# Kernel optimization log

Measured on AMD Instinct MI355X. Metric: run time of the kernel, lower is better.

## Reference

```python
import jax, jax.numpy as jnp
import numpy as np

N, S, D = 4, 2048, 1024
H, HD = 16, 64
DF = 3 * D
EPS = 1e-5

def _layernorm(x, g, b):
    mu = jnp.mean(x, axis=-1, keepdims=True)
    var = jnp.mean((x - mu) ** 2, axis=-1, keepdims=True)
    return (x - mu) * jax.lax.rsqrt(var + EPS) * g + b

def _pos_embed(s, d, dtype):
    pos = jnp.arange(s, dtype=dtype)                      # (S,)
    i = jnp.arange(d, dtype=dtype)                        # (D,)
    ang = pos[:, None] / (10000.0 ** (2.0 * i / d))       # (S,D)
    pe = jnp.where((jnp.arange(d) % 2) == 0, jnp.sin(ang), jnp.cos(ang))
    return pe

def setup_inputs() -> dict:
    key = jax.random.key(0)
    ks = jax.random.split(key, 12)
    def w(k, shape, fan_in):
        return jax.random.normal(k, shape, dtype=jnp.float32) * (fan_in ** -0.5)
    return {
        "x":  jax.random.normal(ks[0], (N, S, D), dtype=jnp.float32),
        "Wq": w(ks[1], (D, H * HD), D),
        "Wk": w(ks[2], (D, H * HD), D),
        "Wv": w(ks[3], (D, H * HD), D),
        "Wo": w(ks[4], (H * HD, D), H * HD),
        "W1": w(ks[5], (D, DF), D),
        "b1": jnp.zeros((DF,), dtype=jnp.float32),
        "W2": w(ks[6], (DF, D), DF),
        "b2": jnp.zeros((D,), dtype=jnp.float32),
        "g1": jnp.ones((D,), dtype=jnp.float32),
        "be1": jnp.zeros((D,), dtype=jnp.float32),
        "g2": jnp.ones((D,), dtype=jnp.float32),
        "be2": jnp.zeros((D,), dtype=jnp.float32),
    }

def reference(x, Wq, Wk, Wv, Wo, W1, b1, W2, b2, g1, be1, g2, be2):
    n, s, d = x.shape
    # positional encoding (added to x; note original scales scores by model_dim**0.5)
    x = x + _pos_embed(s, d, x.dtype)[None, :, :]
    # MHA on norm1(x)
    h = _layernorm(x, g1, be1)
    q = (h @ Wq).reshape(n, s, H, HD)
    k = (h @ Wk).reshape(n, s, H, HD)
    v = (h @ Wv).reshape(n, s, H, HD)
    scores = jnp.einsum('bqhd,bkhd->bhqk', q, k) / jnp.sqrt(jnp.asarray(d, x.dtype))
    attn = jax.nn.softmax(scores, axis=-1)
    o = jnp.einsum('bhqk,bkhd->bqhd', attn, v).reshape(n, s, H * HD)
    x = x + o @ Wo
    # FFN on norm2(x): Linear -> LeakyReLU(0.01) -> Linear (dropout = identity in eval)
    h2 = _layernorm(x, g2, be2)
    f = jax.nn.leaky_relu(h2 @ W1 + b1, negative_slope=0.01)
    x = x + (f @ W2 + b2)
    return x
```

## Files before the change

### kernel.cpp

```cpp
#include <hip/hip_runtime.h>

typedef unsigned short u16;
typedef __bf16 bf16x8 __attribute__((ext_vector_type(8)));
typedef float f32x4 __attribute__((ext_vector_type(4)));

__device__ __forceinline__ u16 f2bf(float f) {
  unsigned u = __builtin_bit_cast(unsigned, f);
  u += 0x7FFFu + ((u >> 16) & 1u);
  return (u16)(u >> 16);
}

#define GLOAD16(g, l) __builtin_amdgcn_global_load_lds( \
    (const __attribute__((address_space(1))) unsigned int*)(const void*)(g), \
    (__attribute__((address_space(3))) unsigned int*)(void*)(l), 16, 0, 0)

#define SW(r, c) (((r) << 6) + ((((c) ^ ((r) & 7))) << 3))

#define QSCALE 0.045084222393f

__global__ __launch_bounds__(256) void tconv(const float* __restrict__ W,
                                             u16* __restrict__ Wt, int K, int N) {
  __shared__ float t[32][33];
  int n0 = blockIdx.x * 32, k0 = blockIdx.y * 32;
  int tx = threadIdx.x, ty = threadIdx.y;
#pragma unroll
  for (int j = 0; j < 4; ++j)
    t[ty + j * 8][tx] = W[(size_t)(k0 + ty + j * 8) * N + n0 + tx];
  __syncthreads();
#pragma unroll
  for (int j = 0; j < 4; ++j)
    Wt[(size_t)(n0 + ty + j * 8) * K + k0 + tx] = f2bf(t[tx][ty + j * 8]);
}

template <bool PE>
__global__ __launch_bounds__(256) void ln_row(const float* __restrict__ in,
                                              const float* __restrict__ g,
                                              const float* __restrict__ be,
                                              float* __restrict__ xout,
                                              u16* __restrict__ hout) {
  const int row = blockIdx.x;
  const int tid = threadIdx.x;
  const int s = row & 2047;
  float4 xv = *(const float4*)&in[(size_t)row * 1024 + tid * 4];
  float vals[4];
  const float* xp = (const float*)&xv;
#pragma unroll
  for (int j = 0; j < 4; ++j) {
    float v = xp[j];
    if (PE) {
      int d = tid * 4 + j;
      float freq = powf(10000.f, -2.f * (float)d * (1.f / 1024.f));
      float ang = (float)s * freq;
      v += (d & 1) ? cosf(ang) : sinf(ang);
    }
    vals[j] = v;
  }
  if (PE) {
    float4 st;
    float* sp = (float*)&st;
#pragma unroll
    for (int j = 0; j < 4; ++j) sp[j] = vals[j];
    *(float4*)&xout[(size_t)row * 1024 + tid * 4] = st;
  }
  float sum = vals[0] + vals[1] + vals[2] + vals[3];
  float sq = vals[0] * vals[0] + vals[1] * vals[1] + vals[2] * vals[2] + vals[3] * vals[3];
#pragma unroll
  for (int d = 1; d < 64; d <<= 1) {
    sum += __shfl_xor(sum, d);
    sq += __shfl_xor(sq, d);
  }
  __shared__ float red[8];
  int wave = tid >> 6, lane = tid & 63;
  if (lane == 0) { red[wave] = sum; red[4 + wave] = sq; }
  __syncthreads();
  sum = red[0] + red[1] + red[2] + red[3];
  sq = red[4] + red[5] + red[6] + red[7];
  float mu = sum * (1.f / 1024.f);
  float var = sq * (1.f / 1024.f) - mu * mu;
  float rv = rsqrtf(var + 1e-5f);
#pragma unroll
  for (int j = 0; j < 4; ++j) {
    int d = tid * 4 + j;
    hout[(size_t)row * 1024 + d] = f2bf((vals[j] - mu) * rv * g[d] + be[d]);
  }
}

#define EPI_QKV 0
#define EPI_OPROJ 1
#define EPI_FFN1 2
#define EPI_FFN2 3

template <int EPI>
__global__ __launch_bounds__(256, 4) void gemm_bt(
    const u16* __restrict__ A, const u16* __restrict__ Bt, int M, int N, int K,
    const float* __restrict__ bias, const float* __restrict__ resid,
    float* __restrict__ outf, u16* __restrict__ outb,
    u16* __restrict__ oq, u16* __restrict__ okk, u16* __restrict__ ovt) {
  __shared__ __align__(16) u16 As[128 * 64];
  __shared__ __align__(16) u16 Bs[128 * 64];
  const int tid = threadIdx.x;
  const int wave = tid >> 6, lane = tid & 63;
  const int m0 = blockIdx.y * 128, n0 = blockIdx.x * 128;
  const int lrow = lane & 15, lhi = lane >> 4;
  const int wr = (wave >> 1) * 64, wc = (wave & 1) * 64;
  const int srow = tid >> 3;
  const int swsrc = ((tid & 7) ^ (srow & 7)) * 8;
  const u16* Ag = A + (size_t)(m0 + srow) * K + swsrc;
  const u16* Bg = Bt + (size_t)(n0 + srow) * K + swsrc;

  f32x4 acc[4][4] = {};

  for (int kt = 0; kt < K; kt += 64) {
#pragma unroll
    for (int j = 0; j < 4; ++j) {
      GLOAD16(Ag + (size_t)(j * 32) * K + kt, &As[j * 2048 + wave * 512]);
      GLOAD16(Bg + (size_t)(j * 32) * K + kt, &Bs[j * 2048 + wave * 512]);
    }
    __syncthreads();
    bf16x8 af[2][4], bfr[2][4];
#pragma unroll
    for (int kk = 0; kk < 2; ++kk) {
#pragma unroll
      for (int m = 0; m < 4; ++m)
        af[kk][m] = *(const bf16x8*)&As[SW(wr + m * 16 + lrow, kk * 4 + lhi)];
#pragma unroll
      for (int n = 0; n < 4; ++n)
        bfr[kk][n] = *(const bf16x8*)&Bs[SW(wc + n * 16 + lrow, kk * 4 + lhi)];
    }
#pragma unroll
    for (int kk = 0; kk < 2; ++kk)
#pragma unroll
      for (int m = 0; m < 4; ++m)
#pragma unroll
        for (int n = 0; n < 4; ++n)
          acc[m][n] = __builtin_amdgcn_mfma_f32_16x16x32_bf16(af[kk][m], bfr[kk][n], acc[m][n], 0, 0, 0);
    __syncthreads();
  }

#pragma unroll
  for (int m = 0; m < 4; ++m) {
#pragma unroll
    for (int n = 0; n < 4; ++n) {
#pragma unroll
      for (int i = 0; i < 4; ++i) {
        int row = m0 + wr + m * 16 + lhi * 4 + i;
        int col = n0 + wc + n * 16 + lrow;
        float v = acc[m][n][i];
        if (EPI == EPI_QKV) {
          int which = col >> 10, c = col & 1023;
          int h = c >> 6, hd = c & 63;
          int b = row >> 11, s = row & 2047;
          size_t qk = (((size_t)(b * 16 + h) * 2048 + s) << 6) + hd;
          if (which == 0) oq[qk] = f2bf(v * QSCALE);
          else if (which == 1) okk[qk] = f2bf(v);
          else ovt[((size_t)(b * 16 + h) * 64 + hd) * 2048 + s] = f2bf(v);
        } else if (EPI == EPI_OPROJ) {
          size_t idx = (size_t)row * 1024 + col;
          outf[idx] = v + resid[idx];
        } else if (EPI == EPI_FFN1) {
          float t = v + bias[col];
          t = t > 0.f ? t : 0.01f * t;
          outb[(size_t)row * 3072 + col] = f2bf(t);
        } else {
          size_t idx = (size_t)row * 1024 + col;
          outf[idx] = v + bias[col] + resid[idx];
        }
      }
    }
  }
}

__global__ __launch_bounds__(256, 3) void attn_fwd(const u16* __restrict__ qb,
                                                   const u16* __restrict__ kbuf,
                                                   const u16* __restrict__ vtb,
                                                   u16* __restrict__ ob) {
  __shared__ __align__(16) u16 Kl[2][64 * 64];
  __shared__ __align__(16) u16 Vl[2][64 * 64];
  __shared__ __align__(16) u16 Pl[128 * 64];
  const int tid = threadIdx.x, wave = tid >> 6, lane = tid & 63;
  const int wid = (blockIdx.x & 7) * 128 + (blockIdx.x >> 3);
  const int bh = wid >> 4, qt = wid & 15;
  const int lrow = lane & 15, lhi = lane >> 4;
  const u16* Qg = qb + (((size_t)bh * 2048 + qt * 128) << 6);
  const u16* Kg = kbuf + ((size_t)bh * 2048 << 6);
  const u16* Vg = vtb + (size_t)bh * 64 * 2048;
  const int srow = tid >> 3;
  const int swsrc = ((tid & 7) ^ (srow & 7)) * 8;

#pragma unroll
  for (int j = 0; j < 4; ++j)
    GLOAD16(Qg + (size_t)(srow + j * 32) * 64 + swsrc, &Pl[j * 2048 + wave * 512]);
#pragma unroll
  for (int j = 0; j < 2; ++j) {
    int r = srow + j * 32;
    GLOAD16(Kg + (size_t)r * 64 + swsrc, &Kl[0][j * 2048 + wave * 512]);
    GLOAD16(Vg + (size_t)r * 2048 + swsrc, &Vl[0][j * 2048 + wave * 512]);
  }
  __syncthreads();

  bf16x8 qf[2][2];
#pragma unroll
  for (int m = 0; m < 2; ++m)
#pragma unroll
    for (int kk = 0; kk < 2; ++kk)
      qf[m][kk] = *(const bf16x8*)&Pl[SW(wave * 32 + m * 16 + lrow, kk * 4 + lhi)];

  f32x4 oacc[2][4] = {};
  float lsum[8];
#pragma unroll
  for (int i = 0; i < 8; ++i) lsum[i] = 0.f;

  int cur = 0;
  for (int kv = 0; kv < 2048; kv += 64) {
    if (kv) __syncthreads();
    if (kv + 64 < 2048) {
#pragma unroll
      for (int j = 0; j < 2; ++j) {
        int r = srow + j * 32;
        GLOAD16(Kg + (size_t)(kv + 64 + r) * 64 + swsrc, &Kl[cur ^ 1][j * 2048 + wave * 512]);
        GLOAD16(Vg + (size_t)r * 2048 + kv + 64 + swsrc, &Vl[cur ^ 1][j * 2048 + wave * 512]);
      }
    }

    f32x4 sf[2][4] = {};
#pragma unroll
    for (int n = 0; n < 4; ++n) {
#pragma unroll
      for (int kk = 0; kk < 2; ++kk) {
        bf16x8 kf = *(const bf16x8*)&Kl[cur][SW(n * 16 + lrow, kk * 4 + lhi)];
        sf[0][n] = __builtin_amdgcn_mfma_f32_16x16x32_bf16(qf[0][kk], kf, sf[0][n], 0, 0, 0);
        sf[1][n] = __builtin_amdgcn_mfma_f32_16x16x32_bf16(qf[1][kk], kf, sf[1][n], 0, 0, 0);
      }
    }
#pragma unroll
    for (int m = 0; m < 2; ++m) {
#pragma unroll
      for (int i = 0; i < 4; ++i) {
        float rs = 0.f;
#pragma unroll
        for (int n = 0; n < 4; ++n) {
          float p = exp2f(sf[m][n][i]);
          sf[m][n][i] = p;
          rs += p;
        }
        lsum[m * 4 + i] += rs;
      }
    }
#pragma unroll
    for (int m = 0; m < 2; ++m)
#pragma unroll
      for (int n = 0; n < 4; ++n)
#pragma unroll
        for (int i = 0; i < 4; ++i) {
          int pr = wave * 32 + m * 16 + lhi * 4 + i;
          Pl[SW(pr, n * 2 + (lrow >> 3)) + (lrow & 7)] = f2bf(sf[m][n][i]);
        }
#pragma unroll
    for (int kk = 0; kk < 2; ++kk) {
      bf16x8 pf0 = *(const bf16x8*)&Pl[SW(wave * 32 + 0 + lrow, kk * 4 + lhi)];
      bf16x8 pf1 = *(const bf16x8*)&Pl[SW(wave * 32 + 16 + lrow, kk * 4 + lhi)];
#pragma unroll
      for (int n = 0; n < 4; ++n) {
        bf16x8 vf = *(const bf16x8*)&Vl[cur][SW(n * 16 + lrow, kk * 4 + lhi)];
        oacc[0][n] = __builtin_amdgcn_mfma_f32_16x16x32_bf16(pf0, vf, oacc[0][n], 0, 0, 0);
        oacc[1][n] = __builtin_amdgcn_mfma_f32_16x16x32_bf16(pf1, vf, oacc[1][n], 0, 0, 0);
      }
    }
    cur ^= 1;
  }

#pragma unroll
  for (int idx = 0; idx < 8; ++idx)
#pragma unroll
    for (int d = 1; d < 16; d <<= 1)
      lsum[idx] += __shfl_xor(lsum[idx], d, 16);

  const int b = bh >> 4, h = bh & 15;
#pragma unroll
  for (int m = 0; m < 2; ++m)
#pragma unroll
    for (int i = 0; i < 4; ++i) {
      int qrow = qt * 128 + wave * 32 + m * 16 + lhi * 4 + i;
      float inv = 1.f / lsum[m * 4 + i];
#pragma unroll
      for (int n = 0; n < 4; ++n) {
        int hd = n * 16 + lrow;
        ob[((size_t)(b * 2048 + qrow)) * 1024 + h * 64 + hd] = f2bf(oacc[m][n][i] * inv);
      }
    }
}

extern "C" void kernel_launch(void* const* d_in, const int* in_sizes, int n_in,
                              void* d_out, int out_size, void* d_ws, size_t ws_size,
                              hipStream_t stream) {
  const float* x = (const float*)d_in[0];
  const float* Wq = (const float*)d_in[1];
  const float* Wk = (const float*)d_in[2];
  const float* Wv = (const float*)d_in[3];
  const float* Wo = (const float*)d_in[4];
  const float* W1 = (const float*)d_in[5];
  const float* b1 = (const float*)d_in[6];
  const float* W2 = (const float*)d_in[7];
  const float* b2 = (const float*)d_in[8];
  const float* g1 = (const float*)d_in[9];
  const float* be1 = (const float*)d_in[10];
  const float* g2 = (const float*)d_in[11];
  const float* be2 = (const float*)d_in[12];

  char* ws = (char*)d_ws;
  const size_t MB = 1024 * 1024;
  float* x1 = (float*)(ws + 0);
  u16* h = (u16*)(ws + 32 * MB);
  u16* q = (u16*)(ws + 48 * MB);
  u16* k = (u16*)(ws + 64 * MB);
  u16* vt = (u16*)(ws + 80 * MB);
  u16* o = (u16*)(ws + 96 * MB);
  u16* f = (u16*)(ws + 48 * MB);
  u16* wqkv = (u16*)(ws + 112 * MB);
  u16* wo = (u16*)(ws + 118 * MB);
  u16* w1t = (u16*)(ws + 120 * MB);
  u16* w2t = (u16*)(ws + 126 * MB);
  float* out = (float*)d_out;

  dim3 tb(32, 8);
  tconv<<<dim3(32, 32), tb, 0, stream>>>(Wq, wqkv, 1024, 1024);
  tconv<<<dim3(32, 32), tb, 0, stream>>>(Wk, wqkv + 1024 * 1024, 1024, 1024);
  tconv<<<dim3(32, 32), tb, 0, stream>>>(Wv, wqkv + 2 * 1024 * 1024, 1024, 1024);
  tconv<<<dim3(32, 32), tb, 0, stream>>>(Wo, wo, 1024, 1024);
  tconv<<<dim3(96, 32), tb, 0, stream>>>(W1, w1t, 1024, 3072);
  tconv<<<dim3(32, 96), tb, 0, stream>>>(W2, w2t, 3072, 1024);

  ln_row<true><<<8192, 256, 0, stream>>>(x, g1, be1, x1, h);

  gemm_bt<EPI_QKV><<<dim3(24, 64), 256, 0, stream>>>(h, wqkv, 8192, 3072, 1024,
                                                     nullptr, nullptr, nullptr, nullptr,
                                                     q, k, vt);
  attn_fwd<<<1024, 256, 0, stream>>>(q, k, vt, o);

  gemm_bt<EPI_OPROJ><<<dim3(8, 64), 256, 0, stream>>>(o, wo, 8192, 1024, 1024,
                                                      nullptr, x1, x1, nullptr,
                                                      nullptr, nullptr, nullptr);
  ln_row<false><<<8192, 256, 0, stream>>>(x1, g2, be2, nullptr, h);

  gemm_bt<EPI_FFN1><<<dim3(24, 64), 256, 0, stream>>>(h, w1t, 8192, 3072, 1024,
                                                      b1, nullptr, nullptr, f,
                                                      nullptr, nullptr, nullptr);
  gemm_bt<EPI_FFN2><<<dim3(8, 64), 256, 0, stream>>>(f, w2t, 8192, 1024, 3072,
                                                     b2, x1, out, nullptr,
                                                     nullptr, nullptr, nullptr);
}
```

Measured before the change: 455.0 us.

## Merge weight transposes into one launch and process two query tiles per attention block

The six weight-transpose launches become a single kernel that picks the matrix from the block index, which cuts launch overhead. The attention kernel now runs 512 blocks that each loop over two query tiles, so fewer workgroups are launched and each stays resident longer. The exp2f with a log2e-folded QSCALE is replaced by __expf with QSCALE set to 1/32, which is the same maths written another way. With only 512 blocks, the attention launch may leave compute units underfilled or unbalanced.

```diff
diff --git a/kernel.cpp b/kernel.cpp
--- a/kernel.cpp
+++ b/kernel.cpp
@@ -16,12 +16,36 @@
 
 #define SW(r, c) (((r) << 6) + ((((c) ^ ((r) & 7))) << 3))
 
-#define QSCALE 0.045084222393f
-
-__global__ __launch_bounds__(256) void tconv(const float* __restrict__ W,
-                                             u16* __restrict__ Wt, int K, int N) {
+#define QSCALE 0.03125f
+
+__global__ __launch_bounds__(256) void tconv_all(
+    const float* __restrict__ Wq, const float* __restrict__ Wk,
+    const float* __restrict__ Wv, const float* __restrict__ Wo,
+    const float* __restrict__ W1, const float* __restrict__ W2,
+    u16* __restrict__ wqkv, u16* __restrict__ wo,
+    u16* __restrict__ w1t, u16* __restrict__ w2t) {
   __shared__ float t[32][33];
-  int n0 = blockIdx.x * 32, k0 = blockIdx.y * 32;
+  const int b = blockIdx.x;
+  const float* W;
+  u16* Wt;
+  int K, N, n0, k0;
+  if (b < 4096) {
+    int which = b >> 10, tt = b & 1023;
+    K = 1024; N = 1024;
+    n0 = (tt & 31) * 32; k0 = (tt >> 5) * 32;
+    W = (which == 0) ? Wq : (which == 1) ? Wk : (which == 2) ? Wv : Wo;
+    Wt = (which < 3) ? (wqkv + (size_t)which * 1024 * 1024) : wo;
+  } else if (b < 7168) {
+    int tt = b - 4096;
+    K = 1024; N = 3072;
+    n0 = (tt % 96) * 32; k0 = (tt / 96) * 32;
+    W = W1; Wt = w1t;
+  } else {
+    int tt = b - 7168;
+    K = 3072; N = 1024;
+    n0 = (tt & 31) * 32; k0 = (tt >> 5) * 32;
+    W = W2; Wt = w2t;
+  }
   int tx = threadIdx.x, ty = threadIdx.y;
 #pragma unroll
   for (int j = 0; j < 4; ++j)
@@ -178,116 +202,121 @@
   __shared__ __align__(16) u16 Vl[2][64 * 64];
   __shared__ __align__(16) u16 Pl[128 * 64];
   const int tid = threadIdx.x, wave = tid >> 6, lane = tid & 63;
-  const int wid = (blockIdx.x & 7) * 128 + (blockIdx.x >> 3);
-  const int bh = wid >> 4, qt = wid & 15;
+  const int wid = (blockIdx.x & 7) * 64 + (blockIdx.x >> 3);
+  const int bh = wid >> 3, qtb = wid & 7;
   const int lrow = lane & 15, lhi = lane >> 4;
-  const u16* Qg = qb + (((size_t)bh * 2048 + qt * 128) << 6);
   const u16* Kg = kbuf + ((size_t)bh * 2048 << 6);
   const u16* Vg = vtb + (size_t)bh * 64 * 2048;
   const int srow = tid >> 3;
   const int swsrc = ((tid & 7) ^ (srow & 7)) * 8;
-
-#pragma unroll
-  for (int j = 0; j < 4; ++j)
-    GLOAD16(Qg + (size_t)(srow + j * 32) * 64 + swsrc, &Pl[j * 2048 + wave * 512]);
-#pragma unroll
-  for (int j = 0; j < 2; ++j) {
-    int r = srow + j * 32;
-    GLOAD16(Kg + (size_t)r * 64 + swsrc, &Kl[0][j * 2048 + wave * 512]);
-    GLOAD16(Vg + (size_t)r * 2048 + swsrc, &Vl[0][j * 2048 + wave * 512]);
-  }
-  __syncthreads();
-
-  bf16x8 qf[2][2];
-#pragma unroll
-  for (int m = 0; m < 2; ++m)
-#pragma unroll
-    for (int kk = 0; kk < 2; ++kk)
-      qf[m][kk] = *(const bf16x8*)&Pl[SW(wave * 32 + m * 16 + lrow, kk * 4 + lhi)];
-
-  f32x4 oacc[2][4] = {};
-  float lsum[8];
-#pragma unroll
-  for (int i = 0; i < 8; ++i) lsum[i] = 0.f;
-
-  int cur = 0;
-  for (int kv = 0; kv < 2048; kv += 64) {
-    if (kv) __syncthreads();
-    if (kv + 64 < 2048) {
-#pragma unroll
-      for (int j = 0; j < 2; ++j) {
-        int r = srow + j * 32;
-        GLOAD16(Kg + (size_t)(kv + 64 + r) * 64 + swsrc, &Kl[cur ^ 1][j * 2048 + wave * 512]);
-        GLOAD16(Vg + (size_t)r * 2048 + kv + 64 + swsrc, &Vl[cur ^ 1][j * 2048 + wave * 512]);
-      }
-    }
-
-    f32x4 sf[2][4] = {};
-#pragma unroll
-    for (int n = 0; n < 4; ++n) {
+  const int b = bh >> 4, h = bh & 15;
+
+  for (int qi = 0; qi < 2; ++qi) {
+    const int qt = qtb + qi * 8;
+    const u16* Qg = qb + (((size_t)bh * 2048 + qt * 128) << 6);
+    if (qi) __syncthreads();
+
+#pragma unroll
+    for (int j = 0; j < 4; ++j)
+      GLOAD16(Qg + (size_t)(srow + j * 32) * 64 + swsrc, &Pl[j * 2048 + wave * 512]);
+#pragma unroll
+    for (int j = 0; j < 2; ++j) {
+      int r = srow + j * 32;
+      GLOAD16(Kg + (size_t)r * 64 + swsrc, &Kl[0][j * 2048 + wave * 512]);
+      GLOAD16(Vg + (size_t)r * 2048 + swsrc, &Vl[0][j * 2048 + wave * 512]);
+    }
+    __syncthreads();
+
+    bf16x8 qf[2][2];
+#pragma unroll
+    for (int m = 0; m < 2; ++m)
+#pragma unroll
+      for (int kk = 0; kk < 2; ++kk)
+        qf[m][kk] = *(const bf16x8*)&Pl[SW(wave * 32 + m * 16 + lrow, kk * 4 + lhi)];
+
+    f32x4 oacc[2][4] = {};
+    float lsum[8];
+#pragma unroll
+    for (int i = 0; i < 8; ++i) lsum[i] = 0.f;
+
+    int cur = 0;
+    for (int kv = 0; kv < 2048; kv += 64) {
+      if (kv) __syncthreads();
+      if (kv + 64 < 2048) {
+#pragma unroll
+        for (int j = 0; j < 2; ++j) {
+          int r = srow + j * 32;
+          GLOAD16(Kg + (size_t)(kv + 64 + r) * 64 + swsrc, &Kl[cur ^ 1][j * 2048 + wave * 512]);
+          GLOAD16(Vg + (size_t)r * 2048 + kv + 64 + swsrc, &Vl[cur ^ 1][j * 2048 + wave * 512]);
+        }
+      }
+
+      f32x4 sf[2][4] = {};
+#pragma unroll
+      for (int n = 0; n < 4; ++n) {
+#pragma unroll
+        for (int kk = 0; kk < 2; ++kk) {
+          bf16x8 kf = *(const bf16x8*)&Kl[cur][SW(n * 16 + lrow, kk * 4 + lhi)];
+          sf[0][n] = __builtin_amdgcn_mfma_f32_16x16x32_bf16(qf[0][kk], kf, sf[0][n], 0, 0, 0);
+          sf[1][n] = __builtin_amdgcn_mfma_f32_16x16x32_bf16(qf[1][kk], kf, sf[1][n], 0, 0, 0);
+        }
+      }
+#pragma unroll
+      for (int m = 0; m < 2; ++m) {
+#pragma unroll
+        for (int i = 0; i < 4; ++i) {
+          float rs = 0.f;
+#pragma unroll
+          for (int n = 0; n < 4; ++n) {
+            float p = __expf(sf[m][n][i]);
+            sf[m][n][i] = p;
+            rs += p;
+          }
+          lsum[m * 4 + i] += rs;
+        }
+      }
+#pragma unroll
+      for (int m = 0; m < 2; ++m)
+#pragma unroll
+        for (int n = 0; n < 4; ++n)
+#pragma unroll
+          for (int i = 0; i < 4; ++i) {
+            int pr = wave * 32 + m * 16 + lhi * 4 + i;
+            Pl[SW(pr, n * 2 + (lrow >> 3)) + (lrow & 7)] = f2bf(sf[m][n][i]);
+          }
 #pragma unroll
       for (int kk = 0; kk < 2; ++kk) {
-        bf16x8 kf = *(const bf16x8*)&Kl[cur][SW(n * 16 + lrow, kk * 4 + lhi)];
-        sf[0][n] = __builtin_amdgcn_mfma_f32_16x16x32_bf16(qf[0][kk], kf, sf[0][n], 0, 0, 0);
-        sf[1][n] = __builtin_amdgcn_mfma_f32_16x16x32_bf16(qf[1][kk], kf, sf[1][n], 0, 0, 0);
-      }
-    }
-#pragma unroll
-    for (int m = 0; m < 2; ++m) {
+        bf16x8 pf0 = *(const bf16x8*)&Pl[SW(wave * 32 + 0 + lrow, kk * 4 + lhi)];
+        bf16x8 pf1 = *(const bf16x8*)&Pl[SW(wave * 32 + 16 + lrow, kk * 4 + lhi)];
+#pragma unroll
+        for (int n = 0; n < 4; ++n) {
+          bf16x8 vf = *(const bf16x8*)&Vl[cur][SW(n * 16 + lrow, kk * 4 + lhi)];
+          oacc[0][n] = __builtin_amdgcn_mfma_f32_16x16x32_bf16(pf0, vf, oacc[0][n], 0, 0, 0);
+          oacc[1][n] = __builtin_amdgcn_mfma_f32_16x16x32_bf16(pf1, vf, oacc[1][n], 0, 0, 0);
+        }
+      }
+      cur ^= 1;
+    }
+
+#pragma unroll
+    for (int idx = 0; idx < 8; ++idx)
+#pragma unroll
+      for (int d = 1; d < 16; d <<= 1)
+        lsum[idx] += __shfl_xor(lsum[idx], d, 16);
+
+#pragma unroll
+    for (int m = 0; m < 2; ++m)
 #pragma unroll
       for (int i = 0; i < 4; ++i) {
-        float rs = 0.f;
+        int qrow = qt * 128 + wave * 32 + m * 16 + lhi * 4 + i;
+        float inv = 1.f / lsum[m * 4 + i];
 #pragma unroll
         for (int n = 0; n < 4; ++n) {
-          float p = exp2f(sf[m][n][i]);
-          sf[m][n][i] = p;
-          rs += p;
-        }
-        lsum[m * 4 + i] += rs;
-      }
-    }
-#pragma unroll
-    for (int m = 0; m < 2; ++m)
-#pragma unroll
-      for (int n = 0; n < 4; ++n)
-#pragma unroll
-        for (int i = 0; i < 4; ++i) {
-          int pr = wave * 32 + m * 16 + lhi * 4 + i;
-          Pl[SW(pr, n * 2 + (lrow >> 3)) + (lrow & 7)] = f2bf(sf[m][n][i]);
-        }
-#pragma unroll
-    for (int kk = 0; kk < 2; ++kk) {
-      bf16x8 pf0 = *(const bf16x8*)&Pl[SW(wave * 32 + 0 + lrow, kk * 4 + lhi)];
-      bf16x8 pf1 = *(const bf16x8*)&Pl[SW(wave * 32 + 16 + lrow, kk * 4 + lhi)];
-#pragma unroll
-      for (int n = 0; n < 4; ++n) {
-        bf16x8 vf = *(const bf16x8*)&Vl[cur][SW(n * 16 + lrow, kk * 4 + lhi)];
-        oacc[0][n] = __builtin_amdgcn_mfma_f32_16x16x32_bf16(pf0, vf, oacc[0][n], 0, 0, 0);
-        oacc[1][n] = __builtin_amdgcn_mfma_f32_16x16x32_bf16(pf1, vf, oacc[1][n], 0, 0, 0);
-      }
-    }
-    cur ^= 1;
-  }
-
-#pragma unroll
-  for (int idx = 0; idx < 8; ++idx)
-#pragma unroll
-    for (int d = 1; d < 16; d <<= 1)
-      lsum[idx] += __shfl_xor(lsum[idx], d, 16);
-
-  const int b = bh >> 4, h = bh & 15;
-#pragma unroll
-  for (int m = 0; m < 2; ++m)
-#pragma unroll
-    for (int i = 0; i < 4; ++i) {
-      int qrow = qt * 128 + wave * 32 + m * 16 + lhi * 4 + i;
-      float inv = 1.f / lsum[m * 4 + i];
-#pragma unroll
-      for (int n = 0; n < 4; ++n) {
-        int hd = n * 16 + lrow;
-        ob[((size_t)(b * 2048 + qrow)) * 1024 + h * 64 + hd] = f2bf(oacc[m][n][i] * inv);
-      }
-    }
+          int hd = n * 16 + lrow;
+          ob[((size_t)(b * 2048 + qrow)) * 1024 + h * 64 + hd] = f2bf(oacc[m][n][i] * inv);
+        }
+      }
+  }
 }
 
 extern "C" void kernel_launch(void* const* d_in, const int* in_sizes, int n_in,
@@ -322,20 +351,15 @@
   u16* w2t = (u16*)(ws + 126 * MB);
   float* out = (float*)d_out;
 
-  dim3 tb(32, 8);
-  tconv<<<dim3(32, 32), tb, 0, stream>>>(Wq, wqkv, 1024, 1024);
-  tconv<<<dim3(32, 32), tb, 0, stream>>>(Wk, wqkv + 1024 * 1024, 1024, 1024);
-  tconv<<<dim3(32, 32), tb, 0, stream>>>(Wv, wqkv + 2 * 1024 * 1024, 1024, 1024);
-  tconv<<<dim3(32, 32), tb, 0, stream>>>(Wo, wo, 1024, 1024);
-  tconv<<<dim3(96, 32), tb, 0, stream>>>(W1, w1t, 1024, 3072);
-  tconv<<<dim3(32, 96), tb, 0, stream>>>(W2, w2t, 3072, 1024);
+  tconv_all<<<10240, dim3(32, 8), 0, stream>>>(Wq, Wk, Wv, Wo, W1, W2,
+                                               wqkv, wo, w1t, w2t);
 
   ln_row<true><<<8192, 256, 0, stream>>>(x, g1, be1, x1, h);
 
   gemm_bt<EPI_QKV><<<dim3(24, 64), 256, 0, stream>>>(h, wqkv, 8192, 3072, 1024,
                                                      nullptr, nullptr, nullptr, nullptr,
                                                      q, k, vt);
-  attn_fwd<<<1024, 256, 0, stream>>>(q, k, vt, o);
+  attn_fwd<<<512, 256, 0, stream>>>(q, k, vt, o);
 
   gemm_bt<EPI_OPROJ><<<dim3(8, 64), 256, 0, stream>>>(o, wo, 8192, 1024, 1024,
                                                       nullptr, x1, x1, nullptr,
```

After: 434.3 us. -4.5%, faster.
